# Optimization experiments

Hardware: AMD Instinct MI355X
Metric: run time of the kernel (lower is better)

The kernel has to match this reference:

```python
import jax, jax.numpy as jnp
import numpy as np
import math

H = 256
NH = 8
HD = H // NH
FF = 2 * H
NSESS = 8
LN_EPS = 1e-5


def _layernorm(x, g, b):
    m = jnp.mean(x, axis=-1, keepdims=True)
    v = jnp.mean((x - m) ** 2, axis=-1, keepdims=True)
    return (x - m) / jnp.sqrt(v + LN_EPS) * g + b


def setup_inputs() -> dict:
    key = jax.random.key(0)
    ks = jax.random.split(key, 32)
    B, S, N = 4, 256, 32
    inp = {
        'sequence': jax.random.normal(ks[0], (B, S, N, H), dtype=jnp.float32),
        'regime_signal': jax.random.normal(ks[1], (B, S), dtype=jnp.float32),
        'session_transition': jax.random.normal(ks[2], (B, S), dtype=jnp.float32),
    }
    w = lambda k, shape: jax.random.normal(k, shape, dtype=jnp.float32) * 0.02
    inp['q_w'] = w(ks[3], (H, H)); inp['q_b'] = jnp.zeros((H,), jnp.float32)
    inp['k_w'] = w(ks[4], (H, H)); inp['k_b'] = jnp.zeros((H,), jnp.float32)
    inp['v_w'] = w(ks[5], (H, H)); inp['v_b'] = jnp.zeros((H,), jnp.float32)
    inp['o_w'] = w(ks[6], (H, H)); inp['o_b'] = jnp.zeros((H,), jnp.float32)
    inp['sess_emb'] = w(ks[7], (NSESS, H))
    inp['reg_w'] = w(ks[8], (H,)); inp['reg_b'] = jnp.zeros((H,), jnp.float32)
    inp['tr_w'] = w(ks[9], (H,)); inp['tr_b'] = jnp.zeros((H,), jnp.float32)
    inp['tq_w'] = w(ks[10], (H, H)); inp['tq_b'] = jnp.zeros((H,), jnp.float32)
    inp['tk_w'] = w(ks[11], (H, H)); inp['tk_b'] = jnp.zeros((H,), jnp.float32)
    inp['ff_w1'] = w(ks[12], (H, FF)); inp['ff_b1'] = jnp.zeros((FF,), jnp.float32)
    inp['ff_w2'] = w(ks[13], (FF, H)); inp['ff_b2'] = jnp.zeros((H,), jnp.float32)
    inp['ln1_g'] = jnp.ones((H,), jnp.float32); inp['ln1_b'] = jnp.zeros((H,), jnp.float32)
    inp['ln2_g'] = jnp.ones((H,), jnp.float32); inp['ln2_b'] = jnp.zeros((H,), jnp.float32)
    inp['valid_mask'] = jax.random.randint(ks[14], (B, S, N), 0, 2).astype(bool)
    inp['session_codes'] = jax.random.randint(ks[15], (B, S), 0, NSESS).astype(jnp.int64)
    return inp


def _forward(sequence, regime_signal, session_transition,
             q_w, q_b, k_w, k_b, v_w, v_b, o_w, o_b,
             sess_emb, reg_w, reg_b, tr_w, tr_b,
             tq_w, tq_b, tk_w, tk_b,
             ff_w1, ff_b1, ff_w2, ff_b2,
             ln1_g, ln1_b, ln2_g, ln2_b,
             valid_mask, session_codes):
    B, S, N, Hd = sequence.shape
    BN = B * N
    # [B,S,N,H] -> [B*N, S, H]
    flat = sequence.transpose(0, 2, 1, 3).reshape(BN, S, Hd)

    # time-state: session embedding + regime/transition scalar projections
    sess = jnp.clip(session_codes, 0, NSESS - 1)
    sess_flat = jnp.broadcast_to(sess[:, None, :], (B, N, S)).reshape(BN, S)
    time_state = sess_emb[sess_flat]  # [BN, S, H]
    reg_flat = jnp.broadcast_to(regime_signal[:, None, :], (B, N, S)).reshape(BN, S)
    time_state = time_state + reg_flat[..., None] * reg_w + reg_b
    tr_flat = jnp.broadcast_to(session_transition[:, None, :], (B, N, S)).reshape(BN, S)
    time_state = time_state + tr_flat[..., None] * tr_w + tr_b

    def heads(x):  # [BN,S,H] -> [BN,NH,S,HD]
        return x.reshape(BN, S, NH, HD).transpose(0, 2, 1, 3)

    q = heads((flat + time_state) @ q_w + q_b)
    k = heads((flat + time_state) @ k_w + k_b)
    v = heads(flat @ v_w + v_b)
    tq = heads(time_state @ tq_w + tq_b)
    tk = heads(time_state @ tk_w + tk_b)

    scale = 1.0 / math.sqrt(float(HD))
    scores = jnp.einsum('bhqd,bhkd->bhqk', q, k) * scale
    scores = scores + 0.25 * jnp.einsum('bhqd,bhkd->bhqk', tq, tk) * scale

    causal = jnp.triu(jnp.ones((S, S), dtype=bool), k=1)
    scores = jnp.where(causal[None, None], -10000.0, scores)

    valid = valid_mask.transpose(0, 2, 1).reshape(BN, S)  # [BN,S]
    all_invalid = ~jnp.any(valid, axis=1)  # [BN]
    scores = jnp.where(~valid[:, None, None, :], -10000.0, scores)
    first_key = (jnp.arange(S) == 0)
    scores = jnp.where(all_invalid[:, None, None, None] & first_key, 0.0, scores)

    attn = jax.nn.softmax(scores, axis=-1)
    attn = attn * valid[:, None, None, :].astype(attn.dtype)
    attn = attn / jnp.maximum(jnp.sum(attn, axis=-1, keepdims=True), 1e-6)
    attn = jnp.where(all_invalid[:, None, None, None], 0.0, attn)

    attn_out = jnp.einsum('bhqk,bhkd->bhqd', attn, v)
    attn_out = attn_out.transpose(0, 2, 1, 3).reshape(BN, S, Hd)
    attn_out = attn_out @ o_w + o_b

    x = _layernorm(flat + attn_out, ln1_g, ln1_b)  # dropout identity (eval / p=0)
    ff = jax.nn.gelu(x @ ff_w1 + ff_b1, approximate=False) @ ff_w2 + ff_b2
    x = _layernorm(x + ff, ln2_g, ln2_b)
    x = x * valid[..., None].astype(x.dtype)
    return x.reshape(B, N, S, Hd).transpose(0, 2, 1, 3)  # [B,S,N,H]


def reference(sequence, regime_signal, session_transition,
              q_w, q_b, k_w, k_b, v_w, v_b, o_w, o_b,
              sess_emb, reg_w, reg_b, tr_w, tr_b,
              tq_w, tq_b, tk_w, tk_b,
              ff_w1, ff_b1, ff_w2, ff_b2,
              ln1_g, ln1_b, ln2_g, ln2_b,
              valid_mask, session_codes):
    return _forward(sequence, regime_signal, session_transition,
                    q_w, q_b, k_w, k_b, v_w, v_b, o_w, o_b,
                    sess_emb, reg_w, reg_b, tr_w, tr_b,
                    tq_w, tq_b, tk_w, tk_b,
                    ff_w1, ff_b1, ff_w2, ff_b2,
                    ln1_g, ln1_b, ln2_g, ln2_b,
                    valid_mask, session_codes)
```

## Files before the change

### kernel.cpp

```cpp
#include <hip/hip_runtime.h>
#include <math.h>

#define B_ 4
#define S_ 256
#define N_ 32
#define H_ 256
#define NH_ 8
#define HD_ 32
#define FF_ 512
#define BN_ 128
#define M_ 32768
#define BS_ 1024

typedef __attribute__((ext_vector_type(8))) short short8;
typedef __attribute__((ext_vector_type(4))) short short4v;
typedef __attribute__((ext_vector_type(4))) float f32x4;
typedef __attribute__((ext_vector_type(16))) float f32x16;
typedef __attribute__((ext_vector_type(4))) int i32x4;

__device__ __forceinline__ unsigned short f2bf(float f) {
  unsigned u = __builtin_bit_cast(unsigned, f);
  u = (u + 0x7FFFu + ((u >> 16) & 1u)) >> 16;
  return (unsigned short)u;
}
__device__ __forceinline__ float bf2f(unsigned short h) {
  unsigned u = ((unsigned)h) << 16;
  return __builtin_bit_cast(float, u);
}

__device__ __forceinline__ void gload16(const void* g, void* l) {
  __builtin_amdgcn_global_load_lds(
      (const __attribute__((address_space(1))) unsigned*)g,
      (__attribute__((address_space(3))) unsigned*)l, 16, 0, 0);
}

__global__ __launch_bounds__(256)
void ts_kernel(const float* __restrict__ reg, const float* __restrict__ tr,
               const int* __restrict__ codes,
               const float* __restrict__ sess_emb,
               const float* __restrict__ reg_w, const float* __restrict__ reg_b,
               const float* __restrict__ tr_w, const float* __restrict__ tr_b,
               float* __restrict__ ts) {
  const int bs = blockIdx.x;
  const int h = threadIdx.x;
  int c = codes[bs];
  c = c < 0 ? 0 : (c > 7 ? 7 : c);
  const float r = reg[bs], t = tr[bs];
  ts[bs * H_ + h] = sess_emb[c * H_ + h] + r * reg_w[h] + reg_b[h]
                    + t * tr_w[h] + tr_b[h];
}

__global__ __launch_bounds__(256)
void cvtall_kernel(const float* __restrict__ q_w, const float* __restrict__ k_w,
                   const float* __restrict__ v_w, const float* __restrict__ o_w,
                   const float* __restrict__ tq_w, const float* __restrict__ tk_w,
                   const float* __restrict__ ff1_w, const float* __restrict__ ff2_w,
                   unsigned short* __restrict__ wqk, unsigned short* __restrict__ wv,
                   unsigned short* __restrict__ wo, unsigned short* __restrict__ wtqtk,
                   unsigned short* __restrict__ wff1, unsigned short* __restrict__ wff2) {
  const int bid = blockIdx.x, tid = threadIdx.x;
  const float* src; unsigned short* dst; int ns, K, base;
  if (bid < 256)       { src = q_w;   dst = wqk;           ns = 8; K = 256; base = 0; }
  else if (bid < 512)  { src = k_w;   dst = wqk + 65536;   ns = 8; K = 256; base = 256; }
  else if (bid < 768)  { src = v_w;   dst = wv;            ns = 8; K = 256; base = 512; }
  else if (bid < 1024) { src = o_w;   dst = wo;            ns = 8; K = 256; base = 768; }
  else if (bid < 1280) { src = tq_w;  dst = wtqtk;         ns = 8; K = 256; base = 1024; }
  else if (bid < 1536) { src = tk_w;  dst = wtqtk + 65536; ns = 8; K = 256; base = 1280; }
  else if (bid < 2048) { src = ff1_w; dst = wff1;          ns = 9; K = 256; base = 1536; }
  else                 { src = ff2_w; dst = wff2;          ns = 8; K = 512; base = 2048; }
  const int idx = (bid - base) * 256 + tid;
  const int k = idx >> ns, n = idx & ((1 << ns) - 1);
  dst[n * K + k] = f2bf(src[idx]);
}

__global__ __launch_bounds__(256)
void prep_kernel(const float* __restrict__ seq, const float* __restrict__ ts,
                 unsigned short* __restrict__ flatb, unsigned short* __restrict__ fpb) {
  const int row = blockIdx.x * 8 + (threadIdx.x >> 5);
  const int c0 = (threadIdx.x & 31) * 8;
  const int bn = row >> 8, s = row & 255;
  const int b = bn >> 5, n = bn & 31;
  const float* sp = &seq[((((b << 8) + s) << 5) + n) * 256 + c0];
  const float* tp = &ts[(((b << 8) + s) << 8) + c0];
  const float4 a0 = *(const float4*)sp, a1 = *(const float4*)(sp + 4);
  const float4 t0 = *(const float4*)tp, t1 = *(const float4*)(tp + 4);
  short8 fv, gv;
  fv[0] = (short)f2bf(a0.x); fv[1] = (short)f2bf(a0.y);
  fv[2] = (short)f2bf(a0.z); fv[3] = (short)f2bf(a0.w);
  fv[4] = (short)f2bf(a1.x); fv[5] = (short)f2bf(a1.y);
  fv[6] = (short)f2bf(a1.z); fv[7] = (short)f2bf(a1.w);
  gv[0] = (short)f2bf(a0.x + t0.x); gv[1] = (short)f2bf(a0.y + t0.y);
  gv[2] = (short)f2bf(a0.z + t0.z); gv[3] = (short)f2bf(a0.w + t0.w);
  gv[4] = (short)f2bf(a1.x + t1.x); gv[5] = (short)f2bf(a1.y + t1.y);
  gv[6] = (short)f2bf(a1.z + t1.z); gv[7] = (short)f2bf(a1.w + t1.w);
  *(short8*)&flatb[row * 256 + c0] = fv;
  *(short8*)&fpb[row * 256 + c0] = gv;
}

template<int AMODE, int RESMODE, bool GELU_, int K, int NOUT, bool OUTBF,
         bool DUALB, bool SCALEH>
__global__ __launch_bounds__(256)
void mmb_kernel(const void* __restrict__ Av, const unsigned short* __restrict__ Wt,
                const float* __restrict__ bias, const float* __restrict__ bias2,
                const unsigned short* __restrict__ resb,
                void* __restrict__ Cv, float post_scale) {
  constexpr int LDA = (AMODE == 3) ? 64 : 72;
  constexpr int LDB = (AMODE == 3) ? 64 : 72;
  __shared__ unsigned short As[128 * 72];
  __shared__ unsigned short Bs[128 * 72];
  const int tid = threadIdx.x;
  const int m0 = blockIdx.x * 128, n0 = blockIdx.y * 128;
  const int l = tid & 63, w = tid >> 6;
  const int wr = w >> 1, wc = w & 1;
  const int lr = l & 15, lg = l >> 4;
  f32x4 acc[4][4] = {};

  const unsigned short* ga = nullptr;
  const unsigned short* gb = nullptr;
  if (AMODE == 3) {
    ga = (const unsigned short*)Av + (m0 + w * 32 + (l >> 3)) * K + (l & 7) * 8;
    gb = Wt + (n0 + w * 32 + (l >> 3)) * K + (l & 7) * 8;
  }

  for (int k0 = 0; k0 < K; k0 += 64) {
    if (AMODE == 3) {
#pragma unroll
      for (int i = 0; i < 4; ++i) {
        gload16(ga + k0 + i * 8 * K, &As[(w * 32 + i * 8) * 64]);
        gload16(gb + k0 + i * 8 * K, &Bs[(w * 32 + i * 8) * 64]);
      }
    } else {
#pragma unroll
      for (int i = 0; i < 8; ++i) {
        const int seg = i * 256 + tid;
        const int r = seg >> 4, c4 = (seg & 15) * 4;
        const float4 a4 = *(const float4*)&((const float*)Av)[(m0 + r) * K + k0 + c4];
        short4v sv;
        sv[0] = (short)f2bf(a4.x); sv[1] = (short)f2bf(a4.y);
        sv[2] = (short)f2bf(a4.z); sv[3] = (short)f2bf(a4.w);
        *(short4v*)&As[r * LDA + c4] = sv;
      }
#pragma unroll
      for (int i = 0; i < 4; ++i) {
        const int seg = i * 256 + tid;
        const int n = seg >> 3, c8 = (seg & 7) * 8;
        const short8 v = *(const short8*)&Wt[(n0 + n) * K + k0 + c8];
        *(short8*)&Bs[n * LDB + c8] = v;
      }
    }
    __syncthreads();
#pragma unroll
    for (int ks = 0; ks < 2; ++ks) {
      short8 af[4], bfr[4];
#pragma unroll
      for (int qt = 0; qt < 4; ++qt)
        af[qt] = *(const short8*)&As[(wr * 64 + qt * 16 + lr) * LDA + ks * 32 + lg * 8];
#pragma unroll
      for (int nt = 0; nt < 4; ++nt)
        bfr[nt] = *(const short8*)&Bs[(wc * 64 + nt * 16 + lr) * LDB + ks * 32 + lg * 8];
#pragma unroll
      for (int qt = 0; qt < 4; ++qt)
#pragma unroll
        for (int nt = 0; nt < 4; ++nt)
          acc[qt][nt] = __builtin_amdgcn_mfma_f32_16x16x32_bf16(
              af[qt], bfr[nt], acc[qt][nt], 0, 0, 0);
    }
    __syncthreads();
  }

#pragma unroll
  for (int qt = 0; qt < 4; ++qt) {
#pragma unroll
    for (int nt = 0; nt < 4; ++nt) {
      const int col = n0 + wc * 64 + nt * 16 + lr;
      const float bsv = DUALB ? (col < 256 ? bias[col] : bias2[col - 256])
                              : bias[col];
      const float sc = SCALEH ? (col < 256 ? post_scale : 1.0f) : post_scale;
#pragma unroll
      for (int i = 0; i < 4; ++i) {
        const int row = m0 + wr * 64 + qt * 16 + (lg << 2) + i;
        float v = (acc[qt][nt][i] + bsv) * sc;
        if (RESMODE == 2) v += bf2f(resb[row * NOUT + col]);
        if (GELU_) v = 0.5f * v * (1.0f + erff(v * 0.70710678118654752f));
        if (OUTBF) ((unsigned short*)Cv)[row * NOUT + col] = f2bf(v);
        else       ((float*)Cv)[row * NOUT + col] = v;
      }
    }
  }
}

template<int K, bool FINAL>
__global__ __launch_bounds__(256, 2)
void gemmln_kernel(const unsigned short* __restrict__ Ab,
                   const unsigned short* __restrict__ Wt,
                   const float* __restrict__ bias,
                   const unsigned short* __restrict__ resb,
                   const float* __restrict__ g, const float* __restrict__ bb,
                   const int* __restrict__ valid,
                   void* __restrict__ out) {
  __shared__ unsigned short As[64 * 64];
  __shared__ unsigned short Bs[256 * 64];
  __shared__ float Red[4][64][2];
  const int tid = threadIdx.x;
  const int m0 = blockIdx.x * 64;
  const int l = tid & 63, w = tid >> 6;
  const int lr = l & 15, lg = l >> 4;
  f32x4 acc[4][4] = {};

  const unsigned short* ga = Ab + (m0 + w * 16 + (l >> 3)) * K + (l & 7) * 8;
  const unsigned short* gb = Wt + (w * 64 + (l >> 3)) * K + (l & 7) * 8;

  for (int k0 = 0; k0 < K; k0 += 64) {
#pragma unroll
    for (int i = 0; i < 2; ++i)
      gload16(ga + k0 + i * 8 * K, &As[(w * 16 + i * 8) * 64]);
#pragma unroll
    for (int i = 0; i < 8; ++i)
      gload16(gb + k0 + i * 8 * K, &Bs[(w * 64 + i * 8) * 64]);
    __syncthreads();
#pragma unroll
    for (int ks = 0; ks < 2; ++ks) {
      short8 af[4], bfr[4];
#pragma unroll
      for (int qt = 0; qt < 4; ++qt)
        af[qt] = *(const short8*)&As[(qt * 16 + lr) * 64 + ks * 32 + lg * 8];
#pragma unroll
      for (int nt = 0; nt < 4; ++nt)
        bfr[nt] = *(const short8*)&Bs[(w * 64 + nt * 16 + lr) * 64 + ks * 32 + lg * 8];
#pragma unroll
      for (int qt = 0; qt < 4; ++qt)
#pragma unroll
        for (int nt = 0; nt < 4; ++nt)
          acc[qt][nt] = __builtin_amdgcn_mfma_f32_16x16x32_bf16(
              af[qt], bfr[nt], acc[qt][nt], 0, 0, 0);
    }
    __syncthreads();
  }

#pragma unroll
  for (int qt = 0; qt < 4; ++qt) {
#pragma unroll
    for (int i = 0; i < 4; ++i) {
      const int rl = qt * 16 + (lg << 2) + i;
      const int row = m0 + rl;
      float s1 = 0.0f, s2 = 0.0f;
#pragma unroll
      for (int nt = 0; nt < 4; ++nt) {
        const int col = w * 64 + nt * 16 + lr;
        float v = acc[qt][nt][i] + bias[col] + bf2f(resb[row * 256 + col]);
        acc[qt][nt][i] = v;
        s1 += v; s2 += v * v;
      }
      s1 += __shfl_xor(s1, 1); s2 += __shfl_xor(s2, 1);
      s1 += __shfl_xor(s1, 2); s2 += __shfl_xor(s2, 2);
      s1 += __shfl_xor(s1, 4); s2 += __shfl_xor(s2, 4);
      s1 += __shfl_xor(s1, 8); s2 += __shfl_xor(s2, 8);
      if (lr == 0) { Red[w][rl][0] = s1; Red[w][rl][1] = s2; }
    }
  }
  __syncthreads();

#pragma unroll
  for (int qt = 0; qt < 4; ++qt) {
#pragma unroll
    for (int i = 0; i < 4; ++i) {
      const int rl = qt * 16 + (lg << 2) + i;
      const int row = m0 + rl;
      const float s1 = (Red[0][rl][0] + Red[1][rl][0])
                     + (Red[2][rl][0] + Red[3][rl][0]);
      const float s2 = (Red[0][rl][1] + Red[1][rl][1])
                     + (Red[2][rl][1] + Red[3][rl][1]);
      const float mean = s1 * (1.0f / 256.0f);
      const float var = s2 * (1.0f / 256.0f) - mean * mean;
      const float rstd = rsqrtf(var + 1e-5f);
      if (FINAL) {
        const int bn = row >> 8, s = row & 255;
        const int b = bn >> 5, n = bn & 31;
        const float vm = (valid[((b << 8) + s) * 32 + n] != 0) ? 1.0f : 0.0f;
        float* op = (float*)out + ((((b << 8) + s) << 5) + n) * 256;
#pragma unroll
        for (int nt = 0; nt < 4; ++nt) {
          const int col = w * 64 + nt * 16 + lr;
          op[col] = ((acc[qt][nt][i] - mean) * rstd * g[col] + bb[col]) * vm;
        }
      } else {
        unsigned short* op = (unsigned short*)out + row * 256;
#pragma unroll
        for (int nt = 0; nt < 4; ++nt) {
          const int col = w * 64 + nt * 16 + lr;
          op[col] = f2bf((acc[qt][nt][i] - mean) * rstd * g[col] + bb[col]);
        }
      }
    }
  }
}

__global__ __launch_bounds__(512, 4)
void attn4_kernel(const unsigned short* __restrict__ qkb,
                  const unsigned short* __restrict__ vb,
                  const unsigned short* __restrict__ tqtkb,
                  const int* __restrict__ valid,
                  unsigned short* __restrict__ ao) {
  __shared__ __align__(16) char KsB[256 * 128];
  __shared__ __align__(16) char VsB[32 * 512];

  const int bn = blockIdx.x & 127;
  const int h = blockIdx.x >> 7;
  const int b = bn >> 5, n = bn & 31;
  const int tid = threadIdx.x, l = tid & 63, w = tid >> 6;
  const int lq = l & 31, hi = l >> 5;
  const int qa = w * 32 + lq;

  const unsigned long long bm0 = __ballot(valid[((b << 8) + 0   + l) * 32 + n] != 0);
  const unsigned long long bm1 = __ballot(valid[((b << 8) + 64  + l) * 32 + n] != 0);
  const unsigned long long bm2 = __ballot(valid[((b << 8) + 128 + l) * 32 + n] != 0);
  const unsigned long long bm3 = __ballot(valid[((b << 8) + 192 + l) * 32 + n] != 0);

  short8 qf[4];
  {
    const unsigned short* qp = &qkb[((bn << 8) + qa) * 512 + (h << 5)];
    const unsigned short* tp = &tqtkb[((b << 8) + qa) * 512 + (h << 5)];
    qf[0] = *(const short8*)&qp[hi * 8];
    qf[1] = *(const short8*)&qp[16 + hi * 8];
    qf[2] = *(const short8*)&tp[hi * 8];
    qf[3] = *(const short8*)&tp[16 + hi * 8];
  }

#pragma unroll
  for (int i = 0; i < 4; ++i) {
    const int e = i * 512 + tid;
    const int key = e >> 3, c = e & 7;
    const unsigned short* src = (c < 4)
        ? &qkb[((bn << 8) + key) * 512 + 256 + (h << 5) + c * 8]
        : &tqtkb[((b << 8) + key) * 512 + 256 + (h << 5) + (c - 4) * 8];
    *(short8*)(KsB + key * 128 + ((c * 16) ^ ((key & 7) << 4))) = *(const short8*)src;
  }
#pragma unroll
  for (int i = 0; i < 2; ++i) {
    const int e = i * 512 + tid;
    const int key = e >> 2, c = e & 3;
    const short8 v = *(const short8*)&vb[((bn << 8) + key) * 256 + (h << 5) + c * 8];
#pragma unroll
    for (int j = 0; j < 8; ++j) {
      const int dv = c * 8 + j;
      *(unsigned short*)(VsB + dv * 512 + ((key * 2) ^ ((dv & 7) << 4))) =
          (unsigned short)v[j];
    }
  }
  __syncthreads();

  f32x16 oacc = {};
  float lrun = 0.0f;

  for (int g = 0; g <= w; ++g) {
    const int kbase = g << 5;
    f32x16 s = {};
#pragma unroll
    for (int df = 0; df < 4; ++df) {
      const int key = kbase + lq;
      const short8 akf = *(const short8*)(
          KsB + key * 128 + ((df * 32 + hi * 16) ^ ((key & 7) << 4)));
      s = __builtin_amdgcn_mfma_f32_32x32x16_bf16(akf, qf[df], s, 0, 0, 0);
    }
    const unsigned long long bmc = (kbase < 64) ? bm0 : (kbase < 128) ? bm1
                                 : (kbase < 192) ? bm2 : bm3;
    const unsigned wnd = (kbase & 32) ? (unsigned)(bmc >> 32) : (unsigned)bmc;
    float p[16];
#pragma unroll
    for (int r = 0; r < 16; ++r) {
      const int crow = (r & 3) + 8 * (r >> 2) + 4 * hi;
      const int key = kbase + crow;
      const bool ok = (key <= qa) && (((wnd >> crow) & 1u) != 0u);
      p[r] = ok ? __builtin_amdgcn_exp2f(s[r]) : 0.0f;
    }
    float rs = ((p[0] + p[1]) + (p[2] + p[3])) + ((p[4] + p[5]) + (p[6] + p[7]))
             + ((p[8] + p[9]) + (p[10] + p[11])) + ((p[12] + p[13]) + (p[14] + p[15]));
    rs += __shfl_xor(rs, 32);
    lrun += rs;
    unsigned wds[8];
#pragma unroll
    for (int i2 = 0; i2 < 8; ++i2)
      wds[i2] = (unsigned)f2bf(p[2 * i2]) | ((unsigned)f2bf(p[2 * i2 + 1]) << 16);
    unsigned xw[8];
#pragma unroll
    for (int i2 = 0; i2 < 8; ++i2)
      xw[i2] = (unsigned)__shfl_xor((int)wds[i2], 32);
    i32x4 f0, f1;
    f0[0] = (int)(hi ? xw[2] : wds[0]);
    f0[1] = (int)(hi ? xw[3] : wds[1]);
    f0[2] = (int)(hi ? wds[2] : xw[0]);
    f0[3] = (int)(hi ? wds[3] : xw[1]);
    f1[0] = (int)(hi ? xw[6] : wds[4]);
    f1[1] = (int)(hi ? xw[7] : wds[5]);
    f1[2] = (int)(hi ? wds[6] : xw[4]);
    f1[3] = (int)(hi ? wds[7] : xw[5]);
    const short8 pf0 = __builtin_bit_cast(short8, f0);
    const short8 pf1 = __builtin_bit_cast(short8, f1);
    {
      const short8 avf = *(const short8*)(
          VsB + lq * 512 + (((kbase + hi * 8) * 2) ^ ((lq & 7) << 4)));
      oacc = __builtin_amdgcn_mfma_f32_32x32x16_bf16(avf, pf0, oacc, 0, 0, 0);
    }
    {
      const short8 avf = *(const short8*)(
          VsB + lq * 512 + (((kbase + 16 + hi * 8) * 2) ^ ((lq & 7) << 4)));
      oacc = __builtin_amdgcn_mfma_f32_32x32x16_bf16(avf, pf1, oacc, 0, 0, 0);
    }
  }

  const float inv = 1.0f / fmaxf(lrun, 1e-6f);
  const int row = (bn << 8) + qa;
#pragma unroll
  for (int g2 = 0; g2 < 4; ++g2) {
    const unsigned long long h0 = f2bf(oacc[4 * g2 + 0] * inv);
    const unsigned long long h1 = f2bf(oacc[4 * g2 + 1] * inv);
    const unsigned long long h2 = f2bf(oacc[4 * g2 + 2] * inv);
    const unsigned long long h3 = f2bf(oacc[4 * g2 + 3] * inv);
    const unsigned long long pkt = h0 | (h1 << 16) | (h2 << 32) | (h3 << 48);
    *(unsigned long long*)&ao[row * 256 + (h << 5) + 8 * g2 + 4 * hi] = pkt;
  }
}

extern "C" void kernel_launch(void* const* d_in, const int* in_sizes, int n_in,
                              void* d_out, int out_size, void* d_ws, size_t ws_size,
                              hipStream_t stream) {
  const float* seq    = (const float*)d_in[0];
  const float* regs   = (const float*)d_in[1];
  const float* trs    = (const float*)d_in[2];
  const float* q_w    = (const float*)d_in[3];
  const float* q_b    = (const float*)d_in[4];
  const float* k_w    = (const float*)d_in[5];
  const float* k_b    = (const float*)d_in[6];
  const float* v_w    = (const float*)d_in[7];
  const float* v_b    = (const float*)d_in[8];
  const float* o_w    = (const float*)d_in[9];
  const float* o_b    = (const float*)d_in[10];
  const float* semb   = (const float*)d_in[11];
  const float* reg_w  = (const float*)d_in[12];
  const float* reg_b  = (const float*)d_in[13];
  const float* tr_w   = (const float*)d_in[14];
  const float* tr_b   = (const float*)d_in[15];
  const float* tq_w   = (const float*)d_in[16];
  const float* tq_b   = (const float*)d_in[17];
  const float* tk_w   = (const float*)d_in[18];
  const float* tk_b   = (const float*)d_in[19];
  const float* ff_w1  = (const float*)d_in[20];
  const float* ff_b1  = (const float*)d_in[21];
  const float* ff_w2  = (const float*)d_in[22];
  const float* ff_b2  = (const float*)d_in[23];
  const float* ln1_g  = (const float*)d_in[24];
  const float* ln1_b  = (const float*)d_in[25];
  const float* ln2_g  = (const float*)d_in[26];
  const float* ln2_b  = (const float*)d_in[27];
  const int*   valid  = (const int*)d_in[28];
  const int*   codes  = (const int*)d_in[29];

  float* f32ws = (float*)d_ws;
  float* ts    = f32ws;
  unsigned short* bws = (unsigned short*)(f32ws + 262144 + 8388608);
  unsigned short* flatb = bws;
  unsigned short* fpb   = bws + 8388608;
  unsigned short* qkb   = bws + 16777216;
  unsigned short* vb    = bws + 33554432;
  unsigned short* tqtkb = bws + 41943040;
  unsigned short* wqk   = bws + 42467328;
  unsigned short* wv    = bws + 42598400;
  unsigned short* wo    = bws + 42663936;
  unsigned short* wtqtk = bws + 42729472;
  unsigned short* wff1  = bws + 42860544;
  unsigned short* wff2  = bws + 42991616;
  unsigned short* ao  = fpb;
  unsigned short* x1b = flatb;
  unsigned short* h1  = qkb;
  float* outp = (float*)d_out;

  const float c2 = 0.25505402f;

  ts_kernel<<<BS_, 256, 0, stream>>>(regs, trs, codes, semb, reg_w, reg_b,
                                     tr_w, tr_b, ts);
  cvtall_kernel<<<2560, 256, 0, stream>>>(q_w, k_w, v_w, o_w, tq_w, tk_w,
                                          ff_w1, ff_w2, wqk, wv, wo, wtqtk,
                                          wff1, wff2);
  prep_kernel<<<M_ / 8, 256, 0, stream>>>(seq, ts, flatb, fpb);
  mmb_kernel<0, 0, false, 256, 512, true, true, true>
      <<<dim3(8, 4), 256, 0, stream>>>(ts, wtqtk, tq_b, tk_b, nullptr,
                                       tqtkb, 0.25f * c2);
  mmb_kernel<3, 0, false, 256, 512, true, true, true>
      <<<dim3(256, 4), 256, 0, stream>>>(fpb, wqk, q_b, k_b, nullptr,
                                         qkb, c2);
  mmb_kernel<3, 0, false, 256, 256, true, false, false>
      <<<dim3(256, 2), 256, 0, stream>>>(flatb, wv, v_b, nullptr, nullptr,
                                         vb, 1.0f);
  attn4_kernel<<<BN_ * NH_, 512, 0, stream>>>(qkb, vb, tqtkb, valid, ao);
  gemmln_kernel<256, false><<<M_ / 64, 256, 0, stream>>>(
      ao, wo, o_b, flatb, ln1_g, ln1_b, nullptr, x1b);
  mmb_kernel<3, 0, true, 256, 512, true, false, false>
      <<<dim3(256, 4), 256, 0, stream>>>(x1b, wff1, ff_b1, nullptr, nullptr,
                                         h1, 1.0f);
  gemmln_kernel<512, true><<<M_ / 64, 256, 0, stream>>>(
      h1, wff2, ff_b2, x1b, ln2_g, ln2_b, valid, outp);
}
```

Baseline: 172.5 us.

## Fuse QKV projection and fold time embedding into per-position bias

Exploits linearity: (x+ts)@W = x@W + ts@W, so the time-session term is projected once per (b,s) with a small GEMM and added as a per-row bias in the QK epilogue. This removes the second bf16 copy of the input (fpb) and lets Q, K and V share one GEMM over a concatenated 768-wide weight, cutting input reads and a launch. The bias is now kept in fp32 instead of being rounded into the bf16 input, which slightly changes numerics. The epilogue gathers the bias by row and column, and attention reads from a 768-stride buffer.

After: 197.5 us. 1.14x slower.

```diff
diff --git a/kernel.cpp b/kernel.cpp
--- a/kernel.cpp
+++ b/kernel.cpp
@@ -55,50 +55,42 @@
                    const float* __restrict__ v_w, const float* __restrict__ o_w,
                    const float* __restrict__ tq_w, const float* __restrict__ tk_w,
                    const float* __restrict__ ff1_w, const float* __restrict__ ff2_w,
-                   unsigned short* __restrict__ wqk, unsigned short* __restrict__ wv,
-                   unsigned short* __restrict__ wo, unsigned short* __restrict__ wtqtk,
+                   unsigned short* __restrict__ wqkv, unsigned short* __restrict__ wo,
+                   unsigned short* __restrict__ wtqtk,
                    unsigned short* __restrict__ wff1, unsigned short* __restrict__ wff2) {
   const int bid = blockIdx.x, tid = threadIdx.x;
   const float* src; unsigned short* dst; int ns, K, base;
-  if (bid < 256)       { src = q_w;   dst = wqk;           ns = 8; K = 256; base = 0; }
-  else if (bid < 512)  { src = k_w;   dst = wqk + 65536;   ns = 8; K = 256; base = 256; }
-  else if (bid < 768)  { src = v_w;   dst = wv;            ns = 8; K = 256; base = 512; }
-  else if (bid < 1024) { src = o_w;   dst = wo;            ns = 8; K = 256; base = 768; }
-  else if (bid < 1280) { src = tq_w;  dst = wtqtk;         ns = 8; K = 256; base = 1024; }
-  else if (bid < 1536) { src = tk_w;  dst = wtqtk + 65536; ns = 8; K = 256; base = 1280; }
-  else if (bid < 2048) { src = ff1_w; dst = wff1;          ns = 9; K = 256; base = 1536; }
-  else                 { src = ff2_w; dst = wff2;          ns = 8; K = 512; base = 2048; }
+  if (bid < 256)       { src = q_w;   dst = wqkv;           ns = 8; K = 256; base = 0; }
+  else if (bid < 512)  { src = k_w;   dst = wqkv + 65536;   ns = 8; K = 256; base = 256; }
+  else if (bid < 768)  { src = v_w;   dst = wqkv + 131072;  ns = 8; K = 256; base = 512; }
+  else if (bid < 1024) { src = o_w;   dst = wo;             ns = 8; K = 256; base = 768; }
+  else if (bid < 1280) { src = tq_w;  dst = wtqtk;          ns = 8; K = 256; base = 1024; }
+  else if (bid < 1536) { src = tk_w;  dst = wtqtk + 65536;  ns = 8; K = 256; base = 1280; }
+  else if (bid < 2048) { src = ff1_w; dst = wff1;           ns = 9; K = 256; base = 1536; }
+  else                 { src = ff2_w; dst = wff2;           ns = 8; K = 512; base = 2048; }
   const int idx = (bid - base) * 256 + tid;
   const int k = idx >> ns, n = idx & ((1 << ns) - 1);
   dst[n * K + k] = f2bf(src[idx]);
 }
 
 __global__ __launch_bounds__(256)
-void prep_kernel(const float* __restrict__ seq, const float* __restrict__ ts,
-                 unsigned short* __restrict__ flatb, unsigned short* __restrict__ fpb) {
+void prep_kernel(const float* __restrict__ seq, unsigned short* __restrict__ flatb) {
   const int row = blockIdx.x * 8 + (threadIdx.x >> 5);
   const int c0 = (threadIdx.x & 31) * 8;
   const int bn = row >> 8, s = row & 255;
   const int b = bn >> 5, n = bn & 31;
   const float* sp = &seq[((((b << 8) + s) << 5) + n) * 256 + c0];
-  const float* tp = &ts[(((b << 8) + s) << 8) + c0];
   const float4 a0 = *(const float4*)sp, a1 = *(const float4*)(sp + 4);
-  const float4 t0 = *(const float4*)tp, t1 = *(const float4*)(tp + 4);
-  short8 fv, gv;
+  short8 fv;
   fv[0] = (short)f2bf(a0.x); fv[1] = (short)f2bf(a0.y);
   fv[2] = (short)f2bf(a0.z); fv[3] = (short)f2bf(a0.w);
   fv[4] = (short)f2bf(a1.x); fv[5] = (short)f2bf(a1.y);
   fv[6] = (short)f2bf(a1.z); fv[7] = (short)f2bf(a1.w);
-  gv[0] = (short)f2bf(a0.x + t0.x); gv[1] = (short)f2bf(a0.y + t0.y);
-  gv[2] = (short)f2bf(a0.z + t0.z); gv[3] = (short)f2bf(a0.w + t0.w);
-  gv[4] = (short)f2bf(a1.x + t1.x); gv[5] = (short)f2bf(a1.y + t1.y);
-  gv[6] = (short)f2bf(a1.z + t1.z); gv[7] = (short)f2bf(a1.w + t1.w);
   *(short8*)&flatb[row * 256 + c0] = fv;
-  *(short8*)&fpb[row * 256 + c0] = gv;
 }
 
 template<int AMODE, int RESMODE, bool GELU_, int K, int NOUT, bool OUTBF,
-         bool DUALB, bool SCALEH>
+         bool DUALB, bool SCALEH, bool QKVE>
 __global__ __launch_bounds__(256)
 void mmb_kernel(const void* __restrict__ Av, const unsigned short* __restrict__ Wt,
                 const float* __restrict__ bias, const float* __restrict__ bias2,
@@ -173,15 +165,27 @@
 #pragma unroll
     for (int nt = 0; nt < 4; ++nt) {
       const int col = n0 + wc * 64 + nt * 16 + lr;
-      const float bsv = DUALB ? (col < 256 ? bias[col] : bias2[col - 256])
-                              : bias[col];
-      const float sc = SCALEH ? (col < 256 ? post_scale : 1.0f) : post_scale;
 #pragma unroll
       for (int i = 0; i < 4; ++i) {
         const int row = m0 + wr * 64 + qt * 16 + (lg << 2) + i;
-        float v = (acc[qt][nt][i] + bsv) * sc;
-        if (RESMODE == 2) v += bf2f(resb[row * NOUT + col]);
-        if (GELU_) v = 0.5f * v * (1.0f + erff(v * 0.70710678118654752f));
+        float v;
+        if (QKVE) {
+          v = acc[qt][nt][i];
+          if (col < 256) v *= post_scale;
+          if (col < 512) {
+            const int bs = (((row >> 13) << 8)) + (row & 255);
+            v += bias[(bs << 9) + col];
+          } else {
+            v += bias2[col - 256 - 256];
+          }
+        } else {
+          const float bsv = DUALB ? (col < 256 ? bias[col] : bias2[col - 256])
+                                  : bias[col];
+          const float sc = SCALEH ? (col < 256 ? post_scale : 1.0f) : post_scale;
+          v = (acc[qt][nt][i] + bsv) * sc;
+          if (RESMODE == 2) v += bf2f(resb[row * NOUT + col]);
+          if (GELU_) v = 0.5f * v * (1.0f + erff(v * 0.70710678118654752f));
+        }
         if (OUTBF) ((unsigned short*)Cv)[row * NOUT + col] = f2bf(v);
         else       ((float*)Cv)[row * NOUT + col] = v;
       }
@@ -296,8 +300,7 @@
 }
 
 __global__ __launch_bounds__(512, 4)
-void attn4_kernel(const unsigned short* __restrict__ qkb,
-                  const unsigned short* __restrict__ vb,
+void attn4_kernel(const unsigned short* __restrict__ qkvb,
                   const unsigned short* __restrict__ tqtkb,
                   const int* __restrict__ valid,
                   unsigned short* __restrict__ ao) {
@@ -318,7 +321,7 @@
 
   short8 qf[4];
   {
-    const unsigned short* qp = &qkb[((bn << 8) + qa) * 512 + (h << 5)];
+    const unsigned short* qp = &qkvb[((bn << 8) + qa) * 768 + (h << 5)];
     const unsigned short* tp = &tqtkb[((b << 8) + qa) * 512 + (h << 5)];
     qf[0] = *(const short8*)&qp[hi * 8];
     qf[1] = *(const short8*)&qp[16 + hi * 8];
@@ -331,7 +334,7 @@
     const int e = i * 512 + tid;
     const int key = e >> 3, c = e & 7;
     const unsigned short* src = (c < 4)
-        ? &qkb[((bn << 8) + key) * 512 + 256 + (h << 5) + c * 8]
+        ? &qkvb[((bn << 8) + key) * 768 + 256 + (h << 5) + c * 8]
         : &tqtkb[((b << 8) + key) * 512 + 256 + (h << 5) + (c - 4) * 8];
     *(short8*)(KsB + key * 128 + ((c * 16) ^ ((key & 7) << 4))) = *(const short8*)src;
   }
@@ -339,7 +342,7 @@
   for (int i = 0; i < 2; ++i) {
     const int e = i * 512 + tid;
     const int key = e >> 2, c = e & 3;
-    const short8 v = *(const short8*)&vb[((bn << 8) + key) * 256 + (h << 5) + c * 8];
+    const short8 v = *(const short8*)&qkvb[((bn << 8) + key) * 768 + 512 + (h << 5) + c * 8];
 #pragma unroll
     for (int j = 0; j < 8; ++j) {
       const int dv = c * 8 + j;
@@ -457,21 +460,19 @@
 
   float* f32ws = (float*)d_ws;
   float* ts    = f32ws;
+  float* tsc   = f32ws + 262144;
   unsigned short* bws = (unsigned short*)(f32ws + 262144 + 8388608);
   unsigned short* flatb = bws;
-  unsigned short* fpb   = bws + 8388608;
-  unsigned short* qkb   = bws + 16777216;
-  unsigned short* vb    = bws + 33554432;
+  unsigned short* ao    = bws + 8388608;
+  unsigned short* qkvb  = bws + 16777216;
   unsigned short* tqtkb = bws + 41943040;
-  unsigned short* wqk   = bws + 42467328;
-  unsigned short* wv    = bws + 42598400;
+  unsigned short* wqkv  = bws + 42467328;
   unsigned short* wo    = bws + 42663936;
   unsigned short* wtqtk = bws + 42729472;
   unsigned short* wff1  = bws + 42860544;
   unsigned short* wff2  = bws + 42991616;
-  unsigned short* ao  = fpb;
   unsigned short* x1b = flatb;
-  unsigned short* h1  = qkb;
+  unsigned short* h1  = qkvb;
   float* outp = (float*)d_out;
 
   const float c2 = 0.25505402f;
@@ -479,22 +480,22 @@
   ts_kernel<<<BS_, 256, 0, stream>>>(regs, trs, codes, semb, reg_w, reg_b,
                                      tr_w, tr_b, ts);
   cvtall_kernel<<<2560, 256, 0, stream>>>(q_w, k_w, v_w, o_w, tq_w, tk_w,
-                                          ff_w1, ff_w2, wqk, wv, wo, wtqtk,
+                                          ff_w1, ff_w2, wqkv, wo, wtqtk,
                                           wff1, wff2);
-  prep_kernel<<<M_ / 8, 256, 0, stream>>>(seq, ts, flatb, fpb);
-  mmb_kernel<0, 0, false, 256, 512, true, true, true>
+  prep_kernel<<<M_ / 8, 256, 0, stream>>>(seq, flatb);
+  mmb_kernel<0, 0, false, 256, 512, false, true, true, false>
+      <<<dim3(8, 4), 256, 0, stream>>>(ts, wqkv, q_b, k_b, nullptr,
+                                       tsc, c2);
+  mmb_kernel<0, 0, false, 256, 512, true, true, true, false>
       <<<dim3(8, 4), 256, 0, stream>>>(ts, wtqtk, tq_b, tk_b, nullptr,
                                        tqtkb, 0.25f * c2);
-  mmb_kernel<3, 0, false, 256, 512, true, true, true>
-      <<<dim3(256, 4), 256, 0, stream>>>(fpb, wqk, q_b, k_b, nullptr,
-                                         qkb, c2);
-  mmb_kernel<3, 0, false, 256, 256, true, false, false>
-      <<<dim3(256, 2), 256, 0, stream>>>(flatb, wv, v_b, nullptr, nullptr,
-                                         vb, 1.0f);
-  attn4_kernel<<<BN_ * NH_, 512, 0, stream>>>(qkb, vb, tqtkb, valid, ao);
+  mmb_kernel<3, 0, false, 256, 768, true, false, false, true>
+      <<<dim3(256, 6), 256, 0, stream>>>(flatb, wqkv, tsc, v_b, nullptr,
+                                         qkvb, c2);
+  attn4_kernel<<<BN_ * NH_, 512, 0, stream>>>(qkvb, tqtkb, valid, ao);
   gemmln_kernel<256, false><<<M_ / 64, 256, 0, stream>>>(
       ao, wo, o_b, flatb, ln1_g, ln1_b, nullptr, x1b);
-  mmb_kernel<3, 0, true, 256, 512, true, false, false>
+  mmb_kernel<3, 0, true, 256, 512, true, false, false, false>
       <<<dim3(256, 4), 256, 0, stream>>>(x1b, wff1, ff_b1, nullptr, nullptr,
                                          h1, 1.0f);
   gemmln_kernel<512, true><<<M_ / 64, 256, 0, stream>>>(
```
